# Kernel tuning notes

Hardware: AMD Instinct MI355X
Metric: run time of the kernel (lower is better)

Reference implementation:

```python
import jax, jax.numpy as jnp
import numpy as np

B, CD, E, H, K, L, NB = 262144, 2, 64, 128, 32, 6, 2
TB = 6.0
MIN_BIN = 1e-3      # nflows DEFAULT_MIN_BIN_WIDTH / HEIGHT
MIN_DERIV = 1e-3    # nflows DEFAULT_MIN_DERIVATIVE
P = 3 * K - 1       # spline params per feature


def _rq_spline(y, uw, uh, ud):
    """Unconstrained rational-quadratic spline (linear tails), forward pass.
    y: [B]; uw, uh: [B,K]; ud: [B,K-1]. Returns (z [B], logabsdet [B])."""
    inside = (y >= -TB) & (y <= TB)
    const = float(np.log(np.exp(1.0 - MIN_DERIV) - 1.0))
    ud = jnp.pad(ud, ((0, 0), (1, 1)), constant_values=const)  # boundary deriv -> 1
    w = jax.nn.softmax(uw, axis=-1)
    w = MIN_BIN + (1.0 - MIN_BIN * K) * w
    cw = jnp.pad(jnp.cumsum(w, -1), ((0, 0), (1, 0)))
    cw = (2.0 * TB) * cw - TB
    cw = cw.at[:, 0].set(-TB).at[:, -1].set(TB)
    w = cw[:, 1:] - cw[:, :-1]
    hgt = jax.nn.softmax(uh, axis=-1)
    hgt = MIN_BIN + (1.0 - MIN_BIN * K) * hgt
    ch = jnp.pad(jnp.cumsum(hgt, -1), ((0, 0), (1, 0)))
    ch = (2.0 * TB) * ch - TB
    ch = ch.at[:, 0].set(-TB).at[:, -1].set(TB)
    hgt = ch[:, 1:] - ch[:, :-1]
    d = MIN_DERIV + jax.nn.softplus(ud)                       # [B,K+1]
    yc = jnp.clip(y, -TB, TB)
    locs = cw.at[:, -1].add(1e-6)                             # nflows searchsorted eps
    idx = jnp.clip(jnp.sum((yc[:, None] >= locs).astype(jnp.int32), -1) - 1, 0, K - 1)
    g = lambda a, i: jnp.take_along_axis(a, i[:, None], axis=1)[:, 0]
    cw_k, w_k = g(cw, idx), g(w, idx)
    ch_k, h_k = g(ch, idx), g(hgt, idx)
    d_k, d_k1 = g(d, idx), g(d, idx + 1)
    s_k = h_k / w_k
    th = (yc - cw_k) / w_k
    th1m = th * (1.0 - th)
    num = h_k * (s_k * th * th + d_k * th1m)
    den = s_k + (d_k + d_k1 - 2.0 * s_k) * th1m
    out = ch_k + num / den
    dnum = s_k * s_k * (d_k1 * th * th + 2.0 * s_k * th1m + d_k * (1.0 - th) ** 2)
    lad = jnp.log(dnum) - 2.0 * jnp.log(den)
    return jnp.where(inside, out, y), jnp.where(inside, lad, 0.0)


def setup_inputs() -> dict:
    key = jax.random.key(0)
    ks = iter(jax.random.split(key, 32))
    w = lambda shape, fan: jax.random.normal(next(ks), shape, jnp.float32) / np.sqrt(fan)
    inp = {
        "y": jax.random.normal(next(ks), (B, 1), jnp.float32),
        "context": jax.random.normal(next(ks), (B, CD), jnp.float32),
        "eW1": w((CD, E), CD), "eb1": jnp.zeros((E,), jnp.float32),
        "eW2": w((E, E), E),   "eb2": jnp.zeros((E,), jnp.float32),
        "eW3": w((E, E), E),   "eb3": jnp.zeros((E,), jnp.float32),
        # per-layer MADE conditioner (input->hidden weight is masked to 0 for features=1)
        "init_b": w((L, H), 1.0),
        "ctx_W": w((L, E, H), E), "ctx_b": jnp.zeros((L, H), jnp.float32),
        "blk_W1": w((L, NB, H, H), H), "blk_b1": jnp.zeros((L, NB, H), jnp.float32),
        "blk_W2": w((L, NB, H, H), H), "blk_b2": jnp.zeros((L, NB, H), jnp.float32),
        "blk_Wc": w((L, NB, E, H), E), "blk_bc": jnp.zeros((L, NB, H), jnp.float32),
        "out_W": w((L, H, P), H), "out_b": jnp.zeros((L, P), jnp.float32),
    }
    return inp


def reference(y, context, eW1, eb1, eW2, eb2, eW3, eb3, init_b, ctx_W, ctx_b,
              blk_W1, blk_b1, blk_W2, blk_b2, blk_Wc, blk_bc, out_W, out_b):
    emb = jax.nn.elu(context @ eW1 + eb1)
    emb = jax.nn.elu(emb @ eW2 + eb2)
    emb = jax.nn.elu(emb @ eW3 + eb3)            # [B,E]
    z = y[:, 0]
    total_lad = jnp.zeros_like(z)
    scale = np.sqrt(H).astype(np.float32)        # nflows divides widths/heights by sqrt(hidden)
    for l in range(L):
        h = init_b[l] + emb @ ctx_W[l] + ctx_b[l]
        for j in range(NB):                       # masked residual blocks (fully open for features=1)
            t = jax.nn.elu(h) @ blk_W1[l, j] + blk_b1[l, j]
            t = jax.nn.elu(t) @ blk_W2[l, j] + blk_b2[l, j]
            gate = jax.nn.sigmoid(emb @ blk_Wc[l, j] + blk_bc[l, j])  # GLU with context
            h = h + t * gate
        p = h @ out_W[l] + out_b[l]               # [B, 3K-1]
        z, lad = _rq_spline(z, p[:, :K] / scale, p[:, K:2 * K] / scale, p[:, 2 * K:])
        total_lad = total_lad + lad
    log_prob = -0.5 * z * z - 0.5 * np.float32(np.log(2.0 * np.pi)) + total_lad
    return log_prob
```

## Files before the change

kernel.cpp:

```cpp
#include <hip/hip_runtime.h>
#include <math.h>

typedef _Float16 hfrag  __attribute__((ext_vector_type(8)));
typedef _Float16 hpack  __attribute__((ext_vector_type(4)));
typedef float    accf   __attribute__((ext_vector_type(16)));

constexpr float cTB = 6.0f;
constexpr float cMB = 0.001f;
constexpr float cMD = 0.001f;

constexpr int SH = 136;
constexpr int SE = 72;
constexpr int SP = 100;

__device__ __forceinline__ float eluf(float x)  { return x > 0.f ? x : __expf(x) - 1.f; }
__device__ __forceinline__ float sigmf(float x) { return 1.f / (1.f + __expf(-x)); }
__device__ __forceinline__ float softplusf_(float x) { return x > 20.f ? x : log1pf(__expf(x)); }

__global__ void prep_frag(const float* __restrict__ src, _Float16* __restrict__ dst,
                          int K, int F, int Fpad, int total) {
  int idx = blockIdx.x * 256 + threadIdx.x;
  if (idx >= total) return;
  const int j    = idx & 7;
  const int lane = (idx >> 3) & 63;
  const int rest = idx >> 9;
  const int csteps = K >> 4;
  const int cstep  = rest % csteps;
  const int rest2  = rest / csteps;
  const int fslices = Fpad >> 5;
  const int fs = rest2 % fslices;
  const int n  = rest2 / fslices;
  const int f  = fs * 32 + (lane & 31);
  const int k  = cstep * 16 + ((lane >> 5) << 3) + j;
  float v = (f < F) ? src[((size_t)n * K + k) * F + f] : 0.f;
  dst[idx] = (_Float16)v;
}

#define GEMM2(WBASE, BPTR, BSTRIDE, KDIM, A0, A1)                              \
  _Pragma("unroll")                                                            \
  for (int c = 0; c < (KDIM); c += 16) {                                       \
    hfrag av = *(const hfrag*)((WBASE) + (c << 5) + lane8);                    \
    hfrag b0 = *(const hfrag*)((BPTR) + col * (BSTRIDE) + c + q8);             \
    hfrag b1 = *(const hfrag*)((BPTR) + (32 + col) * (BSTRIDE) + c + q8);      \
    A0 = __builtin_amdgcn_mfma_f32_32x32x16_f16(av, b0, A0, 0, 0, 0);          \
    A1 = __builtin_amdgcn_mfma_f32_32x32x16_f16(av, b1, A1, 0, 0, 0);          \
  }

__global__ __launch_bounds__(256, 3) void nsf_mfma(
    const float* __restrict__ gy,   const float* __restrict__ gctx,
    const float* __restrict__ eW1,  const float* __restrict__ eb1,
    const float* __restrict__ eb2,  const float* __restrict__ eb3,
    const float* __restrict__ gib,  const float* __restrict__ gcb,
    const float* __restrict__ bb1,  const float* __restrict__ bb2,
    const float* __restrict__ bbc,  const float* __restrict__ gob,
    const _Float16* __restrict__ wE2T, const _Float16* __restrict__ wE3T,
    const _Float16* __restrict__ wCtxT, const _Float16* __restrict__ wW1T,
    const _Float16* __restrict__ wW2T,  const _Float16* __restrict__ wWcT,
    const _Float16* __restrict__ wOutT, float* __restrict__ gout)
{
  __shared__ _Float16 sH[64 * SH];
  __shared__ _Float16 sT[64 * SH];
  __shared__ _Float16 sE[64 * SE];

  const int tid  = threadIdx.x;
  const int wid  = tid >> 6;
  const int lane = tid & 63;
  const int col  = lane & 31;
  const int q    = lane >> 5;
  const int q8   = q * 8;
  const int q4   = q * 4;
  const int f0   = wid * 32;
  const int m0   = blockIdx.x * 64;
  const int lane8 = lane * 8;

  {
    const int m  = tid & 63;
    const int eg = tid >> 6;
    const float2 c2 = *(const float2*)&gctx[(size_t)(m0 + m) * 2];
    #pragma unroll
    for (int j = 0; j < 16; ++j) {
      const int e = eg * 16 + j;
      sH[m * SE + e] = (_Float16)eluf(c2.x * eW1[e] + c2.y * eW1[64 + e] + eb1[e]);
    }
  }
  __syncthreads();
  {
    const int ft = wid & 1, nt = wid >> 1;
    accf a = {};
    const _Float16* wr = wE2T + ft * 2048;
    #pragma unroll
    for (int c = 0; c < 64; c += 16) {
      hfrag av = *(const hfrag*)(wr + (c << 5) + lane8);
      hfrag bv = *(const hfrag*)(&sH[(nt * 32 + col) * SE + c + q8]);
      a = __builtin_amdgcn_mfma_f32_32x32x16_f16(av, bv, a, 0, 0, 0);
    }
    const int mrow = nt * 32 + col;
    #pragma unroll
    for (int g = 0; g < 4; ++g) {
      const int e = 32 * ft + 8 * g + q4;
      const float4 b = *(const float4*)&eb2[e];
      hpack pk;
      #pragma unroll
      for (int r = 0; r < 4; ++r) pk[r] = (_Float16)eluf(a[4 * g + r] + (&b.x)[r]);
      *(hpack*)&sT[mrow * SE + e] = pk;
    }
  }
  __syncthreads();
  {
    const int ft = wid & 1, nt = wid >> 1;
    accf a = {};
    const _Float16* wr = wE3T + ft * 2048;
    #pragma unroll
    for (int c = 0; c < 64; c += 16) {
      hfrag av = *(const hfrag*)(wr + (c << 5) + lane8);
      hfrag bv = *(const hfrag*)(&sT[(nt * 32 + col) * SE + c + q8]);
      a = __builtin_amdgcn_mfma_f32_32x32x16_f16(av, bv, a, 0, 0, 0);
    }
    const int mrow = nt * 32 + col;
    #pragma unroll
    for (int g = 0; g < 4; ++g) {
      const int e = 32 * ft + 8 * g + q4;
      const float4 b = *(const float4*)&eb3[e];
      hpack pk;
      #pragma unroll
      for (int r = 0; r < 4; ++r) pk[r] = (_Float16)eluf(a[4 * g + r] + (&b.x)[r]);
      *(hpack*)&sE[mrow * SE + e] = pk;
    }
  }
  __syncthreads();

  float z = 0.f, lad = 0.f;
  if (tid < 64) z = gy[m0 + tid];

  accf h0, h1;

  for (int l = 0; l < 6; ++l) {
    {
      accf a0 = {}, a1 = {};
      const _Float16* wr = wCtxT + (size_t)l * 8192 + wid * 2048;
      GEMM2(wr, sE, SE, 64, a0, a1)
      #pragma unroll
      for (int nt = 0; nt < 2; ++nt) {
        accf& A = nt ? a1 : a0;
        accf& H = nt ? h1 : h0;
        const int mrow = nt * 32 + col;
        #pragma unroll
        for (int g = 0; g < 4; ++g) {
          const int f = f0 + 8 * g + q4;
          const float4 bi = *(const float4*)&gib[l * 128 + f];
          const float4 bc = *(const float4*)&gcb[l * 128 + f];
          hpack pk;
          #pragma unroll
          for (int r = 0; r < 4; ++r) {
            float hv = A[4 * g + r] + (&bi.x)[r] + (&bc.x)[r];
            H[4 * g + r] = hv;
            pk[r] = (_Float16)eluf(hv);
          }
          *(hpack*)&sH[mrow * SH + f] = pk;
        }
      }
    }
    __syncthreads();

    for (int jb = 0; jb < 2; ++jb) {
      const int wi = l * 2 + jb;
      {
        accf a0 = {}, a1 = {};
        const _Float16* wr = wW1T + (size_t)wi * 16384 + wid * 4096;
        GEMM2(wr, sH, SH, 128, a0, a1)
        #pragma unroll
        for (int nt = 0; nt < 2; ++nt) {
          accf& A = nt ? a1 : a0;
          const int mrow = nt * 32 + col;
          #pragma unroll
          for (int g = 0; g < 4; ++g) {
            const int f = f0 + 8 * g + q4;
            const float4 bv = *(const float4*)&bb1[wi * 128 + f];
            hpack pk;
            #pragma unroll
            for (int r = 0; r < 4; ++r) pk[r] = (_Float16)eluf(A[4 * g + r] + (&bv.x)[r]);
            *(hpack*)&sT[mrow * SH + f] = pk;
          }
        }
      }
      __syncthreads();
      {
        accf a0 = {}, a1 = {}, g0 = {}, g1 = {};
        const _Float16* wr2 = wW2T + (size_t)wi * 16384 + wid * 4096;
        GEMM2(wr2, sT, SH, 128, a0, a1)
        const _Float16* wrc = wWcT + (size_t)wi * 8192 + wid * 2048;
        GEMM2(wrc, sE, SE, 64, g0, g1)
        const bool last = (jb == 1);
        #pragma unroll
        for (int nt = 0; nt < 2; ++nt) {
          accf& A2 = nt ? a1 : a0;
          accf& AG = nt ? g1 : g0;
          accf& H  = nt ? h1 : h0;
          const int mrow = nt * 32 + col;
          #pragma unroll
          for (int g = 0; g < 4; ++g) {
            const int f = f0 + 8 * g + q4;
            const float4 b2v = *(const float4*)&bb2[wi * 128 + f];
            const float4 bcv = *(const float4*)&bbc[wi * 128 + f];
            hpack pk;
            #pragma unroll
            for (int r = 0; r < 4; ++r) {
              const float gate = sigmf(AG[4 * g + r] + (&bcv.x)[r]);
              const float hv = H[4 * g + r] + (A2[4 * g + r] + (&b2v.x)[r]) * gate;
              H[4 * g + r] = hv;
              pk[r] = (_Float16)(last ? hv : eluf(hv));
            }
            *(hpack*)&sH[mrow * SH + f] = pk;
          }
        }
      }
      __syncthreads();
    }

    if (wid < 3) {
      accf a0 = {}, a1 = {};
      const _Float16* wr = wOutT + (size_t)l * 12288 + wid * 4096;
      GEMM2(wr, sH, SH, 128, a0, a1)
      #pragma unroll
      for (int nt = 0; nt < 2; ++nt) {
        accf& A = nt ? a1 : a0;
        const int mrow = nt * 32 + col;
        #pragma unroll
        for (int g = 0; g < 4; ++g) {
          const int f = f0 + 8 * g + q4;
          hpack pk;
          #pragma unroll
          for (int r = 0; r < 4; ++r) {
            const float ob = (f + r < 95) ? gob[l * 95 + f + r] : 0.f;
            pk[r] = (_Float16)(A[4 * g + r] + ob);
          }
          *(hpack*)&sT[mrow * SP + f] = pk;
        }
      }
    }
    __syncthreads();

    if (tid < 64) {
      const float invS = 0.08838834764831845f;
      const _Float16* pmv = &sT[tid * SP];
      auto pm = [&](int i) -> float { return (float)pmv[i]; };
      float mw = pm(0), mh = pm(32);
      #pragma unroll
      for (int i = 1; i < 32; ++i) {
        mw = fmaxf(mw, pm(i));
        mh = fmaxf(mh, pm(32 + i));
      }
      float sw = 0.f, sh = 0.f;
      #pragma unroll
      for (int i = 0; i < 32; ++i) {
        sw += __expf((pm(i) - mw) * invS);
        sh += __expf((pm(32 + i) - mh) * invS);
      }
      const float cw_scale = (1.0f - cMB * 32.f) / sw;
      const float ch_scale = (1.0f - cMB * 32.f) / sh;
      const float yc = fminf(fmaxf(z, -cTB), cTB);

      int idx = 0;
      float cum = 0.f, cw_k = -cTB, cw_k1 = cTB;
      bool take = true;
      #pragma unroll
      for (int i = 1; i <= 32; ++i) {
        float cwi;
        if (i < 32) {
          cum += cMB + __expf((pm(i - 1) - mw) * invS) * cw_scale;
          cwi = 2.f * cTB * cum - cTB;
        } else {
          cwi = cTB;
        }
        if (take) { cw_k1 = cwi; take = false; }
        if (i < 32 && yc >= cwi) { idx = i; cw_k = cwi; take = true; }
      }

      cum = 0.f;
      float ch_k = -cTB, ch_k1 = cTB;
      #pragma unroll
      for (int i = 1; i < 32; ++i) {
        cum += cMB + __expf((pm(32 + i - 1) - mh) * invS) * ch_scale;
        const float chi = 2.f * cTB * cum - cTB;
        if (i == idx) ch_k = chi;
        if (i == idx + 1) ch_k1 = chi;
      }

      const float w_k = cw_k1 - cw_k;
      const float h_k = ch_k1 - ch_k;
      const float d_k  = (idx == 0)  ? 1.f : cMD + softplusf_(pm(64 + idx - 1));
      const float d_k1 = (idx == 31) ? 1.f : cMD + softplusf_(pm(64 + idx));

      const float s_k  = h_k / w_k;
      const float th   = (yc - cw_k) / w_k;
      const float th1m = th * (1.f - th);
      const float numv = h_k * (s_k * th * th + d_k * th1m);
      const float denv = s_k + (d_k + d_k1 - 2.f * s_k) * th1m;
      const float outv = ch_k + numv / denv;
      const float omt  = 1.f - th;
      const float dnum = s_k * s_k * (d_k1 * th * th + 2.f * s_k * th1m + d_k * omt * omt);
      const float ladv = __logf(dnum) - 2.f * __logf(denv);
      const bool inside = (z >= -cTB) && (z <= cTB);
      if (inside) { z = outv; lad += ladv; }
    }
  }

  if (tid < 64) {
    gout[m0 + tid] = -0.5f * z * z - 0.9189385332046727f + lad;
  }
}

extern "C" void kernel_launch(void* const* d_in, const int* in_sizes, int n_in,
                              void* d_out, int out_size, void* d_ws, size_t ws_size,
                              hipStream_t stream) {
  const float* gy   = (const float*)d_in[0];
  const float* gctx = (const float*)d_in[1];
  const float* eW1  = (const float*)d_in[2];
  const float* eb1  = (const float*)d_in[3];
  const float* eW2  = (const float*)d_in[4];
  const float* eb2  = (const float*)d_in[5];
  const float* eW3  = (const float*)d_in[6];
  const float* eb3  = (const float*)d_in[7];
  const float* gib  = (const float*)d_in[8];
  const float* gcW  = (const float*)d_in[9];
  const float* gcb  = (const float*)d_in[10];
  const float* bW1  = (const float*)d_in[11];
  const float* bb1  = (const float*)d_in[12];
  const float* bW2  = (const float*)d_in[13];
  const float* bb2  = (const float*)d_in[14];
  const float* bWc  = (const float*)d_in[15];
  const float* bbc  = (const float*)d_in[16];
  const float* goW  = (const float*)d_in[17];
  const float* gob  = (const float*)d_in[18];

  _Float16* ws    = (_Float16*)d_ws;
  _Float16* wE2T  = ws;
  _Float16* wE3T  = wE2T + 4096;
  _Float16* wCtxT = wE3T + 4096;
  _Float16* wW1T  = wCtxT + 49152;
  _Float16* wW2T  = wW1T + 196608;
  _Float16* wWcT  = wW2T + 196608;
  _Float16* wOutT = wWcT + 98304;

  auto prep = [&](const float* s, _Float16* d, int K, int F, int Fp, int n) {
    int tot = n * Fp * K;
    prep_frag<<<(tot + 255) / 256, 256, 0, stream>>>(s, d, K, F, Fp, tot);
  };
  prep(eW2, wE2T, 64, 64, 64, 1);
  prep(eW3, wE3T, 64, 64, 64, 1);
  prep(gcW, wCtxT, 64, 128, 128, 6);
  prep(bW1, wW1T, 128, 128, 128, 12);
  prep(bW2, wW2T, 128, 128, 128, 12);
  prep(bWc, wWcT, 64, 128, 128, 12);
  prep(goW, wOutT, 128, 95, 96, 6);

  nsf_mfma<<<dim3(262144 / 64), dim3(256), 0, stream>>>(
      gy, gctx, eW1, eb1, eb2, eb3, gib, gcb, bb1, bb2, bbc, gob,
      wE2T, wE3T, wCtxT, wW1T, wW2T, wWcT, wOutT, (float*)d_out);
}
```

Baseline: 931.8 us.

## Hold embedding fragments in registers, drop sE buffer, raise occupancy

The context embedding's MFMA B-fragments are loaded once from shared memory into registers. The shared sE buffer is removed and the ctx and gate GEMMs read those register fragments instead of LDS. Launch bounds go from 3 to 4 blocks per SM, and the gate sigmoid is computed first and kept packed as fp16 so the gate accumulators are freed before the W2 GEMM. This cuts LDS traffic and aims for higher occupancy, but adds register pressure and rounds the gate to fp16.

```diff
diff --git a/kernel.cpp b/kernel.cpp
--- a/kernel.cpp
+++ b/kernel.cpp
@@ -46,7 +46,15 @@
     A1 = __builtin_amdgcn_mfma_f32_32x32x16_f16(av, b1, A1, 0, 0, 0);          \
   }
 
-__global__ __launch_bounds__(256, 3) void nsf_mfma(
+#define GEMM2R(WBASE, A0, A1)                                                  \
+  _Pragma("unroll")                                                            \
+  for (int ci = 0; ci < 4; ++ci) {                                             \
+    hfrag av = *(const hfrag*)((WBASE) + (ci << 9) + lane8);                   \
+    A0 = __builtin_amdgcn_mfma_f32_32x32x16_f16(av, embA[ci], A0, 0, 0, 0);    \
+    A1 = __builtin_amdgcn_mfma_f32_32x32x16_f16(av, embB[ci], A1, 0, 0, 0);    \
+  }
+
+__global__ __launch_bounds__(256, 4) void nsf_mfma(
     const float* __restrict__ gy,   const float* __restrict__ gctx,
     const float* __restrict__ eW1,  const float* __restrict__ eb1,
     const float* __restrict__ eb2,  const float* __restrict__ eb3,
@@ -60,7 +68,6 @@
 {
   __shared__ _Float16 sH[64 * SH];
   __shared__ _Float16 sT[64 * SH];
-  __shared__ _Float16 sE[64 * SE];
 
   const int tid  = threadIdx.x;
   const int wid  = tid >> 6;
@@ -124,8 +131,16 @@
       hpack pk;
       #pragma unroll
       for (int r = 0; r < 4; ++r) pk[r] = (_Float16)eluf(a[4 * g + r] + (&b.x)[r]);
-      *(hpack*)&sE[mrow * SE + e] = pk;
-    }
+      *(hpack*)&sH[mrow * SE + e] = pk;
+    }
+  }
+  __syncthreads();
+
+  hfrag embA[4], embB[4];
+  #pragma unroll
+  for (int ci = 0; ci < 4; ++ci) {
+    embA[ci] = *(const hfrag*)&sH[col * SE + ci * 16 + q8];
+    embB[ci] = *(const hfrag*)&sH[(32 + col) * SE + ci * 16 + q8];
   }
   __syncthreads();
 
@@ -134,11 +149,12 @@
 
   accf h0, h1;
 
+  #pragma unroll 1
   for (int l = 0; l < 6; ++l) {
     {
       accf a0 = {}, a1 = {};
       const _Float16* wr = wCtxT + (size_t)l * 8192 + wid * 2048;
-      GEMM2(wr, sE, SE, 64, a0, a1)
+      GEMM2R(wr, a0, a1)
       #pragma unroll
       for (int nt = 0; nt < 2; ++nt) {
         accf& A = nt ? a1 : a0;
@@ -162,6 +178,7 @@
     }
     __syncthreads();
 
+    #pragma unroll 1
     for (int jb = 0; jb < 2; ++jb) {
       const int wi = l * 2 + jb;
       {
@@ -185,28 +202,41 @@
       }
       __syncthreads();
       {
-        accf a0 = {}, a1 = {}, g0 = {}, g1 = {};
+        hpack gpk[2][4];
+        {
+          accf g0 = {}, g1 = {};
+          const _Float16* wrc = wWcT + (size_t)wi * 8192 + wid * 2048;
+          GEMM2R(wrc, g0, g1)
+          #pragma unroll
+          for (int nt = 0; nt < 2; ++nt) {
+            accf& AG = nt ? g1 : g0;
+            #pragma unroll
+            for (int g = 0; g < 4; ++g) {
+              const int f = f0 + 8 * g + q4;
+              const float4 bcv = *(const float4*)&bbc[wi * 128 + f];
+              #pragma unroll
+              for (int r = 0; r < 4; ++r)
+                gpk[nt][g][r] = (_Float16)sigmf(AG[4 * g + r] + (&bcv.x)[r]);
+            }
+          }
+        }
+        accf a0 = {}, a1 = {};
         const _Float16* wr2 = wW2T + (size_t)wi * 16384 + wid * 4096;
         GEMM2(wr2, sT, SH, 128, a0, a1)
-        const _Float16* wrc = wWcT + (size_t)wi * 8192 + wid * 2048;
-        GEMM2(wrc, sE, SE, 64, g0, g1)
         const bool last = (jb == 1);
         #pragma unroll
         for (int nt = 0; nt < 2; ++nt) {
           accf& A2 = nt ? a1 : a0;
-          accf& AG = nt ? g1 : g0;
           accf& H  = nt ? h1 : h0;
           const int mrow = nt * 32 + col;
           #pragma unroll
           for (int g = 0; g < 4; ++g) {
             const int f = f0 + 8 * g + q4;
             const float4 b2v = *(const float4*)&bb2[wi * 128 + f];
-            const float4 bcv = *(const float4*)&bbc[wi * 128 + f];
             hpack pk;
             #pragma unroll
             for (int r = 0; r < 4; ++r) {
-              const float gate = sigmf(AG[4 * g + r] + (&bcv.x)[r]);
-              const float hv = H[4 * g + r] + (A2[4 * g + r] + (&b2v.x)[r]) * gate;
+              const float hv = H[4 * g + r] + (A2[4 * g + r] + (&b2v.x)[r]) * (float)gpk[nt][g][r];
               H[4 * g + r] = hv;
               pk[r] = (_Float16)(last ? hv : eluf(hv));
             }
```

After: 1.180 ms. +26.6%, slower.
